# Kernel tuning notes

Hardware: AMD Instinct MI355X
Metric: run time of the kernel (lower is better)

Reference implementation:

```python
import jax, jax.numpy as jnp
import numpy as np

GAMMA, RHO, OMEGA = 0.7, 2.0, 0.5
EPS = 1e-6


def setup_inputs() -> dict:
    key = jax.random.key(0)
    S, T, N = 64, 256, 1024
    ks = jax.random.split(key, 7)
    x0 = jax.random.normal(ks[0], (N, 1), dtype=jnp.float32)
    # strictly increasing interaction times so dt > 0
    t = jnp.cumsum(jax.random.uniform(ks[1], (S, T), dtype=jnp.float32) + 0.1, axis=1)
    speed = jax.random.uniform(ks[2], (S, 1, 1, 1), dtype=jnp.float32) + 0.1
    vola = jax.random.uniform(ks[3], (S, 1, 1, 1), dtype=jnp.float32) + 0.1
    adj = (jax.random.uniform(ks[4], (N, N)) < 32.0 / N).astype(jnp.float32)
    noise = jax.random.normal(ks[5], (S, T - 1, N, 1), dtype=jnp.float32)
    items = jax.random.randint(ks[6], (S, T), 0, N)
    return {"x0": x0, "t": t, "speed": speed, "vola": vola,
            "adj": adj, "noise": noise, "items": items}


def _simulate(x0, t, speed, vola, adj, noise, items):
    S, T = t.shape
    N = x0.shape[0]
    dt = jnp.diff(t, axis=1)[:, :, None, None]                     # [S,T-1,1,1]
    # OU std: sqrt(vola^2 * (1 - exp(-2*speed*dt)) / (2*speed + 1e-6))
    scale = jnp.sqrt(vola * vola * (1.0 - jnp.exp(-2.0 * speed * dt))
                     / (2.0 * speed + 1e-6))                       # [S,T-1,1,1]
    noisy = noise * scale                                          # [S,T-1,N,1]

    adj_t = adj.T
    in_deg = adj_t.sum(axis=1)[None, :, None]                      # [1,N,1]
    has_in = in_deg > 0

    seq = jnp.arange(S)
    feat0 = jnp.zeros((S, N, 3), jnp.float32)
    feat0 = feat0.at[seq, items[:, 0], 0].add(1.0)
    feat0 = feat0.at[seq, items[:, 0], 2].add(1.0)
    x_init = jnp.broadcast_to(x0[None], (S, N, 1)).astype(jnp.float32)
    sp = speed[:, 0]                                               # [S,1,1]

    def step(carry, inp):
        x_prev, feat = carry
        dt_i, noisy_i, item_i = inp                                # [S,1,1],[S,N,1],[S]
        agg = jnp.einsum('mn,snk->smk', adj_t, x_prev)             # neighbor sum
        empower = jnp.where(has_in, GAMMA * agg / (in_deg + 1e-7), 0.0)
        stable = (feat[..., 1:2] / (feat[..., 0:1] + EPS)) ** RHO
        level = OMEGA * empower + (1.0 - OMEGA) * stable
        e = jnp.exp(-sp * dt_i)
        x_i = x_prev * e + (1.0 - e) * level + noisy_i
        cur_perf = jax.nn.sigmoid(x_i[seq, item_i, 0])
        success = (cur_perf >= 0.5).astype(jnp.float32)
        feat = feat.at[seq, item_i, 0].add(1.0)
        feat = feat.at[seq, item_i, 1].add(success)
        return (x_i, feat), x_i

    xs = (jnp.moveaxis(dt, 1, 0), jnp.moveaxis(noisy, 1, 0), items[:, 1:].T)
    (_, _), ys = jax.lax.scan(step, (x_init, feat0), xs)
    x = jnp.concatenate([x_init[:, None], jnp.moveaxis(ys, 0, 1)], axis=1)  # [S,T,N,1]
    return x


def reference(x0, t, speed, vola, adj, noise, items):
    return _simulate(x0, t, speed, vola, adj, noise, items)
```

## Files before the change

### kernel.cpp

```cpp
#include <hip/hip_runtime.h>

#define NN 1024
#define TT 256
#define MAXDEG 96

typedef unsigned short u16;
typedef unsigned long long ull;


__device__ __forceinline__ int bofsB(int v) {
    int h = (v >> 5) & 31;
    return 1024 + ((v & ~31) | ((v & 31) ^ h));
}
__device__ __forceinline__ int bofsC(int v) {
    int h = (v >> 5) & 31;
    return 2048 + ((v & ~31) | ((v & 31) ^ ((13 * h + 5) & 31)));
}
__device__ __forceinline__ int cnt_res(int pd, int res) {
    return (pd > res) ? (((pd - 1 - res) >> 5) + 1) : 0;
}
__device__ __forceinline__ int pd_of(int deg) {
    int cap = deg < MAXDEG ? deg : MAXDEG;
    int pd = (cap + 15) & ~7;
    if (pd < 16) pd = 16;
    if (pd > MAXDEG) pd = MAXDEG;
    return pd;
}

__global__ __launch_bounds__(1024) void p1_fill(const float* __restrict__ adj,
                                                u16* __restrict__ nbrC,
                                                int* __restrict__ deg)
{
    __shared__ int cnt_s[16][65];
    const int nl = threadIdx.x & 63;
    const int ch = threadIdx.x >> 6;
    const int n  = blockIdx.x * 64 + nl;

    int c = 0;
    for (int j = 0; j < 64; ++j)
        c += (adj[(ch * 64 + j) * NN + n] != 0.0f) ? 1 : 0;
    cnt_s[ch][nl] = c;
    __syncthreads();

    int pos = 0;
    for (int cc = 0; cc < ch; ++cc) pos += cnt_s[cc][nl];
    if (ch == 15) deg[n] = pos + c;

    for (int j = 0; j < 64; ++j) {
        int mrow = ch * 64 + j;
        if (adj[mrow * NN + n] != 0.0f) {
            if (pos < MAXDEG) nbrC[n * MAXDEG + pos] = (u16)mrow;
            ++pos;
        }
    }
}

__global__ __launch_bounds__(1024) void p2_rank(const int* __restrict__ deg,
                                                int* __restrict__ rank_of,
                                                int* __restrict__ node_of)
{
    __shared__ int pd_s[NN];
    const int n = threadIdx.x;
    int my = pd_of(deg[n]);
    pd_s[n] = my;
    __syncthreads();
    int r = 0;
    for (int m = 0; m < NN; ++m) {
        int pm = pd_s[m];
        r += (pm > my) || (pm == my && m < n);
    }
    rank_of[n] = r;
    node_of[r] = n;
}

__device__ __forceinline__ int reloc_one(ull& freep, int pd, int l, int r, int tl,
                                         int vo, u16 (*who_s)[64],
                                         u16* __restrict__ nbr8, int& maxk)
{
    int ob0 = vo & 31, oh = (vo >> 5) & 31;
    int r0 = (ob0 - l) & 31;
    int r1 = ((ob0 ^ oh) - l) & 31;
    int r2 = ((ob0 ^ ((13 * oh + 5) & 31)) - l) & 31;
    int f0 = (int)((freep >> (2 * r0)) & 3);
    int f1 = (int)((freep >> (2 * r1)) & 3);
    int f2 = (int)((freep >> (2 * r2)) & 3);
    int ro, fo, ow;
    if (f0 > 0)      { ro = r0; fo = f0; ow = vo; }
    else if (f1 > 0) { ro = r1; fo = f1; ow = bofsB(vo); }
    else if (f2 > 0) { ro = r2; fo = f2; ow = bofsC(vo); }
    else return 0;
    int k2 = ro + 32 * (cnt_res(pd, ro) - fo);
    freep -= 1ull << (2 * ro);
    nbr8[((k2 >> 3) << 13) + (r << 3) + (k2 & 7)] = (u16)(ow * 4);
    who_s[k2][tl] = (u16)vo;
    if (k2 > maxk) maxk = k2;
    return 1;
}

__global__ __launch_bounds__(64) void p3_sched(const u16* __restrict__ nbrC,
                                               const int* __restrict__ deg,
                                               const int* __restrict__ rank_of,
                                               u16* __restrict__ nbr8,
                                               int* __restrict__ ngrp_r,
                                               float* __restrict__ invd_r)
{
    __shared__ u16 who_s[MAXDEG][64];
    const int tl = threadIdx.x;
    const int n  = blockIdx.x * 64 + tl;
    const int r  = rank_of[n];
    const int l  = r & 63;
    const int dg = deg[n];
    const int cap = dg < MAXDEG ? dg : MAXDEG;
    const int pd = pd_of(dg);

    ull freep = 0;
    for (int res = 0; res < 32; ++res)
        freep |= (ull)cnt_res(pd, res) << (2 * res);
    for (int k = 0; k < pd; ++k) who_s[k][tl] = 0xFFFF;

    for (int g = 0; g < (pd >> 3); ++g) {
        uint4 pk;
        unsigned w0 = (unsigned)((3072 + ((l + g * 8 + 0) & 31)) * 4);
        unsigned w1 = (unsigned)((3072 + ((l + g * 8 + 1) & 31)) * 4);
        unsigned w2 = (unsigned)((3072 + ((l + g * 8 + 2) & 31)) * 4);
        unsigned w3 = (unsigned)((3072 + ((l + g * 8 + 3) & 31)) * 4);
        unsigned w4 = (unsigned)((3072 + ((l + g * 8 + 4) & 31)) * 4);
        unsigned w5 = (unsigned)((3072 + ((l + g * 8 + 5) & 31)) * 4);
        unsigned w6 = (unsigned)((3072 + ((l + g * 8 + 6) & 31)) * 4);
        unsigned w7 = (unsigned)((3072 + ((l + g * 8 + 7) & 31)) * 4);
        pk.x = w0 | (w1 << 16);
        pk.y = w2 | (w3 << 16);
        pk.z = w4 | (w5 << 16);
        pk.w = w6 | (w7 << 16);
        *(uint4*)(nbr8 + (g << 13) + (r << 3)) = pk;
    }

    const uint4* __restrict__ row = (const uint4*)(nbrC + n * MAXDEG);
    int maxk = 15;

#define EMIT(K, WORD) nbr8[(((K) >> 3) << 13) + (r << 3) + ((K) & 7)] = (u16)((WORD) * 4)

    for (int c8 = 0; c8 < (cap + 7) / 8; ++c8) {
        uint4 w = row[c8];
        int id0 = w.x & 0xFFFF, id1 = w.x >> 16, id2 = w.y & 0xFFFF, id3 = w.y >> 16;
        int id4 = w.z & 0xFFFF, id5 = w.z >> 16, id6 = w.w & 0xFFFF, id7 = w.w >> 16;
        int rk[8];
        rk[0] = rank_of[id0]; rk[1] = rank_of[id1];
        rk[2] = rank_of[id2]; rk[3] = rank_of[id3];
        rk[4] = rank_of[id4]; rk[5] = rank_of[id5];
        rk[6] = rank_of[id6]; rk[7] = rank_of[id7];

        int lim = cap - c8 * 8; if (lim > 8) lim = 8;
        #pragma unroll
        for (int u = 0; u < 8; ++u) {
            if (u >= lim) break;
            int v = rk[u];
            int b0 = v & 31;
            int h  = (v >> 5) & 31;
            int res0 = (b0 - l) & 31;
            int res1 = ((b0 ^ h) - l) & 31;
            int res2 = ((b0 ^ ((13 * h + 5) & 31)) - l) & 31;
            int f0 = (int)((freep >> (2 * res0)) & 3);
            int f1 = (int)((freep >> (2 * res1)) & 3);
            int f2 = (int)((freep >> (2 * res2)) & 3);
            int resw, fw, word;
            if (f0 > 0 && f0 >= f1 && f0 >= f2) {
                resw = res0; fw = f0; word = v;
            } else if (f1 > 0 && f1 >= f2) {
                resw = res1; fw = f1; word = bofsB(v);
            } else if (f2 > 0) {
                resw = res2; fw = f2; word = bofsC(v);
            } else {
                fw = 0; resw = 0; word = v;
            }
            if (fw > 0) {
                int kslot = resw + 32 * (cnt_res(pd, resw) - fw);
                freep -= 1ull << (2 * resw);
                EMIT(kslot, word);
                who_s[kslot][tl] = (u16)v;
                if (kslot > maxk) maxk = kslot;
            } else {
                int done = 0;
                if (cnt_res(pd, res0) > 0) {
                    int vo = who_s[res0][tl];
                    if (vo != 0xFFFF &&
                        reloc_one(freep, pd, l, r, tl, vo, who_s, nbr8, maxk)) {
                        EMIT(res0, v);
                        who_s[res0][tl] = (u16)v;
                        if (res0 > maxk) maxk = res0;
                        done = 1;
                    }
                }
                if (!done && cnt_res(pd, res1) > 0) {
                    int vo = who_s[res1][tl];
                    if (vo != 0xFFFF &&
                        reloc_one(freep, pd, l, r, tl, vo, who_s, nbr8, maxk)) {
                        EMIT(res1, bofsB(v));
                        who_s[res1][tl] = (u16)v;
                        if (res1 > maxk) maxk = res1;
                        done = 1;
                    }
                }
                if (!done && cnt_res(pd, res2) > 0) {
                    int vo = who_s[res2][tl];
                    if (vo != 0xFFFF &&
                        reloc_one(freep, pd, l, r, tl, vo, who_s, nbr8, maxk)) {
                        EMIT(res2, bofsC(v));
                        who_s[res2][tl] = (u16)v;
                        if (res2 > maxk) maxk = res2;
                        done = 1;
                    }
                }
                if (!done) {
                    for (int res = 0; res < 32; ++res) {
                        int f = (int)((freep >> (2 * res)) & 3);
                        if (f > 0) {
                            int kslot = res + 32 * (cnt_res(pd, res) - f);
                            freep -= 1ull << (2 * res);
                            EMIT(kslot, v);
                            who_s[kslot][tl] = (u16)v;
                            if (kslot > maxk) maxk = kslot;
                            break;
                        }
                    }
                }
            }
        }
    }
#undef EMIT
    ngrp_r[r] = (maxk >> 3) + 1;
    invd_r[r] = 0.35f / ((float)dg + 1e-7f);
}

#define LDS_BARRIER() asm volatile("s_waitcnt lgkmcnt(0)\n\ts_barrier" ::: "memory")

__global__ __launch_bounds__(1024) void sim_kernel(
    const float* __restrict__ x0, const float* __restrict__ t,
    const float* __restrict__ speed, const float* __restrict__ vola,
    const float* __restrict__ noise, const int* __restrict__ items,
    const u16* __restrict__ nbr8, const int* __restrict__ node_of,
    const int* __restrict__ rank_of,
    const int* __restrict__ ngrp_r, const float* __restrict__ invd_r,
    float* __restrict__ out)
{
    __shared__ float xb[2][3104];
    __shared__ float4 cst[TT - 1];

    const int s   = blockIdx.x;
    const int tid = threadIdx.x;

    const float sp = speed[s];
    const float vo = vola[s];

    if (tid < TT - 1) {
        float t0 = t[s * TT + tid], t1 = t[s * TT + tid + 1];
        float dt = t1 - t0;
        float e  = expf(-sp * dt);
        float sc = vo * sqrtf((1.0f - e * e) / (2.0f * sp + 1e-6f));
        int   it = items[s * TT + tid + 1];
        cst[tid] = make_float4(e, sc, __int_as_float(it), 0.0f);
    }

    const int   m     = node_of[tid];
    const int   r_out = rank_of[tid];
    const int   wB    = bofsB(tid);
    const int   wC    = bofsC(tid);

    const float x0m = x0[m];
    xb[0][tid] = x0m;
    xb[0][wB]  = x0m;
    xb[0][wC]  = x0m;
    if (tid < 32) { xb[0][3072 + tid] = 0.0f; xb[1][3072 + tid] = 0.0f; }

    float* __restrict__ outp = out + (size_t)s * TT * NN + tid;
    outp[0] = x0[tid];

    const int   ng   = ngrp_r[tid];
    const float invd = invd_r[tid];
    const int   item0 = items[s * TT];
    float a_f = (m == item0) ? 1.0f : 0.0f;
    float s_f = 0.0f;

    const float* __restrict__ nzm = noise + (size_t)s * (TT - 1) * NN + m;
    float nzA = nzm[0];
    float nzB = nzm[NN];

    const uint4* __restrict__ nb = (const uint4*)nbr8 + tid;
    uint4 q0  = nb[0];
    uint4 q1  = nb[1024];
    uint4 q2  = nb[2048];
    uint4 q3  = nb[3072];
    uint4 q4  = nb[4096];
    uint4 q5  = nb[5120];
    uint4 q6  = nb[6144];
    uint4 q7  = nb[7168];
    uint4 q8  = nb[8192];
    uint4 q9  = nb[9216];
    uint4 q10 = nb[10240];
    uint4 q11 = nb[11264];

    __syncthreads();

    float x_own = x0m;

#define G8(V)                                                   \
    acc += *(const float*)(xc + ((V).x & 0xFFFFu));             \
    acc += *(const float*)(xc + ((V).x >> 16));                 \
    acc += *(const float*)(xc + ((V).y & 0xFFFFu));             \
    acc += *(const float*)(xc + ((V).y >> 16));                 \
    acc += *(const float*)(xc + ((V).z & 0xFFFFu));             \
    acc += *(const float*)(xc + ((V).z >> 16));                 \
    acc += *(const float*)(xc + ((V).w & 0xFFFFu));             \
    acc += *(const float*)(xc + ((V).w >> 16));

    for (int i = 0; i < TT - 1; ++i) {
        const float* __restrict__ src = xb[i & 1];
        float* __restrict__ dst       = xb[(i + 1) & 1];
        const float4 c = cst[i];

        int ipre = (i + 2 < TT - 1) ? (i + 2) : (TT - 2);
        float nz_new = nzm[(size_t)ipre * NN];

        float xi_lin = src[r_out];

        float acc = 0.0f;
        const char* xc = (const char*)src;
        G8(q0); G8(q1);
        if (ng > 2) { G8(q2);
        if (ng > 3) { G8(q3);
        if (ng > 4) { G8(q4);
        if (ng > 5) { G8(q5);
        if (ng > 6) { G8(q6);
        if (ng > 7) { G8(q7);
        if (ng > 8) { G8(q8);
        if (ng > 9) { G8(q9);
        if (ng > 10){ G8(q10);
        if (ng > 11){ G8(q11); } } } } } } } } } }

        float nz = nzA * c.y;
        float r  = s_f / (a_f + 1e-6f);
        float level = fmaf(acc, invd, 0.5f * r * r);
        float xn = fmaf(x_own, c.x, fmaf(1.0f - c.x, level, nz));

        dst[tid] = xn;
        dst[wB]  = xn;
        dst[wC]  = xn;
        if (i) outp[(size_t)i * NN] = xi_lin;

        if (m == __float_as_int(c.z)) {
            a_f += 1.0f;
            s_f += (xn >= 0.0f) ? 1.0f : 0.0f;
        }
        x_own = xn;
        nzA = nzB; nzB = nz_new;
        LDS_BARRIER();
    }
#undef G8

    outp[(size_t)(TT - 1) * NN] = xb[1][r_out];
}

extern "C" void kernel_launch(void* const* d_in, const int* in_sizes, int n_in,
                              void* d_out, int out_size, void* d_ws, size_t ws_size,
                              hipStream_t stream)
{
    const float* x0    = (const float*)d_in[0];
    const float* t     = (const float*)d_in[1];
    const float* speed = (const float*)d_in[2];
    const float* vola  = (const float*)d_in[3];
    const float* adj   = (const float*)d_in[4];
    const float* noise = (const float*)d_in[5];
    const int*   items = (const int*)d_in[6];
    float* out = (float*)d_out;

    char* ws = (char*)d_ws;
    int*   deg      = (int*)ws;
    int*   rank_of  = (int*)(ws + 4096);
    int*   node_of  = (int*)(ws + 8192);
    int*   ngrp_r   = (int*)(ws + 12288);
    float* invd_r   = (float*)(ws + 16384);
    u16*   nbrC     = (u16*)(ws + 20480);
    u16*   nbr8     = (u16*)(ws + 20480 + 196608);

    p1_fill<<<16, 1024, 0, stream>>>(adj, nbrC, deg);
    p2_rank<<<1, 1024, 0, stream>>>(deg, rank_of, node_of);
    p3_sched<<<16, 64, 0, stream>>>(nbrC, deg, rank_of, nbr8, ngrp_r, invd_r);
    sim_kernel<<<64, 1024, 0, stream>>>(x0, t, speed, vola, noise, items,
                                        nbr8, node_of, rank_of, ngrp_r, invd_r, out);
}
```

Measured before the change: 415.7 us.

## Split adjacency preprocessing into wider count/rank/fill kernels and index scheduling by rank

Preprocessing moves from one 16-block fill kernel to a count kernel over 256 small blocks, a combined degree-sum and rank kernel, and a separate 256-block fill kernel. This spreads the adjacency scan across more CUs. The scheduling kernel now iterates over rank order (node_of) instead of node order, so each block handles a contiguous rank group with lane equal to thread index. The cost is an extra kernel launch and a second pass over adj. The main simulation kernel is unchanged, so any gain comes only from the preprocessing stages.

```diff
diff --git a/kernel.cpp b/kernel.cpp
--- a/kernel.cpp
+++ b/kernel.cpp
@@ -27,41 +27,29 @@
     return pd;
 }
 
-__global__ __launch_bounds__(1024) void p1_fill(const float* __restrict__ adj,
-                                                u16* __restrict__ nbrC,
-                                                int* __restrict__ deg)
-{
-    __shared__ int cnt_s[16][65];
-    const int nl = threadIdx.x & 63;
-    const int ch = threadIdx.x >> 6;
-    const int n  = blockIdx.x * 64 + nl;
-
+__global__ __launch_bounds__(64) void k1_count(const float* __restrict__ adj,
+                                               int* __restrict__ cnt_part)
+{
+    int tid = blockIdx.x * 64 + threadIdx.x;
+    int chunk = tid >> 10;
+    int n = tid & 1023;
     int c = 0;
     for (int j = 0; j < 64; ++j)
-        c += (adj[(ch * 64 + j) * NN + n] != 0.0f) ? 1 : 0;
-    cnt_s[ch][nl] = c;
-    __syncthreads();
-
-    int pos = 0;
-    for (int cc = 0; cc < ch; ++cc) pos += cnt_s[cc][nl];
-    if (ch == 15) deg[n] = pos + c;
-
-    for (int j = 0; j < 64; ++j) {
-        int mrow = ch * 64 + j;
-        if (adj[mrow * NN + n] != 0.0f) {
-            if (pos < MAXDEG) nbrC[n * MAXDEG + pos] = (u16)mrow;
-            ++pos;
-        }
-    }
-}
-
-__global__ __launch_bounds__(1024) void p2_rank(const int* __restrict__ deg,
-                                                int* __restrict__ rank_of,
-                                                int* __restrict__ node_of)
+        c += (adj[(chunk * 64 + j) * NN + n] != 0.0f) ? 1 : 0;
+    cnt_part[chunk * NN + n] = c;
+}
+
+__global__ __launch_bounds__(1024) void k23_rank(const int* __restrict__ cnt_part,
+                                                 int* __restrict__ deg,
+                                                 int* __restrict__ rank_of,
+                                                 int* __restrict__ node_of)
 {
     __shared__ int pd_s[NN];
     const int n = threadIdx.x;
-    int my = pd_of(deg[n]);
+    int tot = 0;
+    for (int c = 0; c < 16; ++c) tot += cnt_part[c * NN + n];
+    deg[n] = tot;
+    int my = pd_of(tot);
     pd_s[n] = my;
     __syncthreads();
     int r = 0;
@@ -71,6 +59,24 @@
     }
     rank_of[n] = r;
     node_of[r] = n;
+}
+
+__global__ __launch_bounds__(64) void k4_fill(const float* __restrict__ adj,
+                                              const int* __restrict__ cnt_part,
+                                              u16* __restrict__ nbrC)
+{
+    int tid = blockIdx.x * 64 + threadIdx.x;
+    int chunk = tid >> 10;
+    int n = tid & 1023;
+    int pos = 0;
+    for (int c = 0; c < chunk; ++c) pos += cnt_part[c * NN + n];
+    for (int j = 0; j < 64; ++j) {
+        int m = chunk * 64 + j;
+        if (adj[m * NN + n] != 0.0f) {
+            if (pos < MAXDEG) nbrC[n * MAXDEG + pos] = (u16)m;
+            ++pos;
+        }
+    }
 }
 
 __device__ __forceinline__ int reloc_one(ull& freep, int pd, int l, int r, int tl,
@@ -100,15 +106,16 @@
 __global__ __launch_bounds__(64) void p3_sched(const u16* __restrict__ nbrC,
                                                const int* __restrict__ deg,
                                                const int* __restrict__ rank_of,
+                                               const int* __restrict__ node_of,
                                                u16* __restrict__ nbr8,
                                                int* __restrict__ ngrp_r,
                                                float* __restrict__ invd_r)
 {
     __shared__ u16 who_s[MAXDEG][64];
     const int tl = threadIdx.x;
-    const int n  = blockIdx.x * 64 + tl;
-    const int r  = rank_of[n];
-    const int l  = r & 63;
+    const int r  = blockIdx.x * 64 + tl;
+    const int n  = node_of[r];
+    const int l  = tl;
     const int dg = deg[n];
     const int cap = dg < MAXDEG ? dg : MAXDEG;
     const int pd = pd_of(dg);
@@ -374,17 +381,19 @@
     float* out = (float*)d_out;
 
     char* ws = (char*)d_ws;
-    int*   deg      = (int*)ws;
-    int*   rank_of  = (int*)(ws + 4096);
-    int*   node_of  = (int*)(ws + 8192);
-    int*   ngrp_r   = (int*)(ws + 12288);
-    float* invd_r   = (float*)(ws + 16384);
-    u16*   nbrC     = (u16*)(ws + 20480);
-    u16*   nbr8     = (u16*)(ws + 20480 + 196608);
-
-    p1_fill<<<16, 1024, 0, stream>>>(adj, nbrC, deg);
-    p2_rank<<<1, 1024, 0, stream>>>(deg, rank_of, node_of);
-    p3_sched<<<16, 64, 0, stream>>>(nbrC, deg, rank_of, nbr8, ngrp_r, invd_r);
+    int*   cnt_part = (int*)ws;
+    int*   deg      = (int*)(ws + 65536);
+    int*   rank_of  = (int*)(ws + 65536 + 4096);
+    int*   node_of  = (int*)(ws + 65536 + 8192);
+    int*   ngrp_r   = (int*)(ws + 65536 + 12288);
+    float* invd_r   = (float*)(ws + 65536 + 16384);
+    u16*   nbrC     = (u16*)(ws + 65536 + 20480);
+    u16*   nbr8     = (u16*)(ws + 65536 + 20480 + 196608);
+
+    k1_count<<<256, 64, 0, stream>>>(adj, cnt_part);
+    k23_rank<<<1, 1024, 0, stream>>>(cnt_part, deg, rank_of, node_of);
+    k4_fill<<<256, 64, 0, stream>>>(adj, cnt_part, nbrC);
+    p3_sched<<<16, 64, 0, stream>>>(nbrC, deg, rank_of, node_of, nbr8, ngrp_r, invd_r);
     sim_kernel<<<64, 1024, 0, stream>>>(x0, t, speed, vola, noise, items,
                                         nbr8, node_of, rank_of, ngrp_r, invd_r, out);
 }
```

Result: no change. 410.7 us (-1.2%).
